# Performance work log

Hardware: AMD Instinct MI355X
Metric: run time of the kernel (lower is better)

## Reference

```python
import jax, jax.numpy as jnp
import numpy as np

B, T, INPUT_DIM = 4, 2048, 1024
N_HEADS, HEAD_DIM, EMB_DIM = 16, 64, 1024


def setup_inputs() -> dict:
    key = jax.random.key(0)
    ks = jax.random.split(key, 7)
    s = 0.02
    return {
        "k": jax.random.normal(ks[0], (B, T, INPUT_DIM), jnp.float32),
        "q": jax.random.normal(ks[1], (B, T, INPUT_DIM), jnp.float32),
        "v": jax.random.normal(ks[2], (B, T, INPUT_DIM), jnp.float32),
        # weights stored [in, out] (torch Linear applies x @ W.T with W [out,in])
        "w_key": jax.random.normal(ks[3], (INPUT_DIM, N_HEADS * HEAD_DIM), jnp.float32) * s,
        "w_query": jax.random.normal(ks[4], (INPUT_DIM, N_HEADS * HEAD_DIM), jnp.float32) * s,
        "w_value": jax.random.normal(ks[5], (INPUT_DIM, N_HEADS * HEAD_DIM), jnp.float32) * s,
        "w_proj": jax.random.normal(ks[6], (N_HEADS * HEAD_DIM, EMB_DIM), jnp.float32) * s,
    }


def reference(k, q, v, w_key, w_query, w_value, w_proj):
    temperature = np.sqrt(HEAD_DIM).astype(np.float32)
    # projections -> [B, T, H, D]
    kh = (k @ w_key).reshape(B, T, N_HEADS, HEAD_DIM)
    qh = (q @ w_query).reshape(B, T, N_HEADS, HEAD_DIM)
    vh = (v @ w_value).reshape(B, T, N_HEADS, HEAD_DIM)
    # scaled dot-product attention: scores [B, H, T, T]
    scores = jnp.einsum("bqhd,bkhd->bhqk", qh, kh) / temperature
    attn = jax.nn.softmax(scores, axis=-1)
    out = jnp.einsum("bhqk,bkhd->bqhd", attn, vh).reshape(B, T, N_HEADS * HEAD_DIM)
    return out @ w_proj
```

## Files before the change

### kernel.cpp

```cpp
#include <hip/hip_runtime.h>

typedef unsigned short bf16_t;
typedef __attribute__((ext_vector_type(8))) short short8;
typedef __attribute__((ext_vector_type(4))) float f32x4;
typedef __attribute__((ext_vector_type(16))) float f32x16;
typedef __attribute__((ext_vector_type(4))) unsigned short usx4;

#define T_SEQ 2048
#define NHEAD 16

__device__ __forceinline__ unsigned short f2bf(float x) {
  union { float f; unsigned u; } v; v.f = x;
  unsigned r = v.u + 0x7fffu + ((v.u >> 16) & 1u);
  return (unsigned short)(r >> 16);
}

__device__ __forceinline__ void gld_lds16(const void* g, void* l) {
  __builtin_amdgcn_global_load_lds((const __attribute__((address_space(1))) void*)g,
                                   (__attribute__((address_space(3))) void*)l, 16, 0, 0);
}

__device__ __forceinline__ unsigned cvtpk(float lo, float hi) {
  unsigned r;
  asm("v_cvt_pk_bf16_f32 %0, %1, %2" : "=v"(r) : "v"(lo), "v"(hi));
  return r;
}

__global__ __launch_bounds__(256) void cvt3(const float* __restrict__ a,
                                            const float* __restrict__ b,
                                            const float* __restrict__ c,
                                            bf16_t* __restrict__ oa,
                                            bf16_t* __restrict__ ob,
                                            bf16_t* __restrict__ oc, int n4seg) {
  int i = blockIdx.x * 256 + threadIdx.x;
  const int stride = gridDim.x * 256;
  const int total = 3 * n4seg;
  for (; i < total; i += stride) {
    const int seg = i / n4seg;
    const int j = i - seg * n4seg;
    const float* in = (seg == 0) ? a : (seg == 1) ? b : c;
    bf16_t* out = (seg == 0) ? oa : (seg == 1) ? ob : oc;
    const float4 v = ((const float4*)in)[j];
    usx4 w = { f2bf(v.x), f2bf(v.y), f2bf(v.z), f2bf(v.w) };
    ((usx4*)out)[j] = w;
  }
}

__global__ __launch_bounds__(256) void wtrans(const float* __restrict__ w0, const float* __restrict__ w1,
                                              const float* __restrict__ w2, const float* __restrict__ w3,
                                              bf16_t* __restrict__ wt) {
  __shared__ float tile[32][33];
  const float* w = (blockIdx.z == 0) ? w0 : (blockIdx.z == 1) ? w1 : (blockIdx.z == 2) ? w2 : w3;
  bf16_t* o = wt + (size_t)blockIdx.z * 1024 * 1024;
  const int c = threadIdx.x & 31;
  const int r = threadIdx.x >> 5;
  const int k0 = blockIdx.y * 32, n0 = blockIdx.x * 32;
#pragma unroll
  for (int rr = 0; rr < 32; rr += 8)
    tile[r + rr][c] = w[(size_t)(k0 + r + rr) * 1024 + n0 + c];
  __syncthreads();
#pragma unroll
  for (int rr = 0; rr < 32; rr += 8)
    o[(size_t)(n0 + r + rr) * 1024 + k0 + c] = f2bf(tile[c][r + rr]);
}

__global__ __launch_bounds__(256) void gemm_qkv(const bf16_t* __restrict__ A0,
                                                const bf16_t* __restrict__ A1,
                                                const bf16_t* __restrict__ A2,
                                                const bf16_t* __restrict__ Wt,
                                                bf16_t* __restrict__ C0,
                                                bf16_t* __restrict__ C1,
                                                bf16_t* __restrict__ C2) {
  __shared__ bf16_t As[2][128 * 64];
  __shared__ bf16_t Bs[2][128 * 64];
  const int K = 1024;
  const int z = blockIdx.z;
  const bf16_t* A  = (z == 0) ? A0 : (z == 1) ? A1 : A2;
  const bf16_t* Bt = Wt + (size_t)z * 1024 * 1024;
  const int tid = threadIdx.x;
  const int lane = tid & 63;
  const int l15 = lane & 15;
  const int g = lane >> 4;
  const int wave = tid >> 6;
  const int wr = wave >> 1, wc = wave & 1;
  const int f = blockIdx.x + (int)gridDim.x * blockIdx.y;
  const int fp = (f & 7) * 64 + (f >> 3);
  const int col0 = (fp & 7) * 128, row0 = (fp >> 3) * 128;

  f32x4 acc[4][4];
#pragma unroll
  for (int m = 0; m < 4; ++m)
#pragma unroll
    for (int n = 0; n < 4; ++n) acc[m][n] = (f32x4){0.f, 0.f, 0.f, 0.f};

  const int r_st = tid >> 3;
  const int c_st = tid & 7;

  auto stage = [&](int kt, int bi) {
#pragma unroll
    for (int i = 0; i < 4; ++i) {
      const int r = r_st + i * 32;
      gld_lds16(A  + (size_t)(row0 + r) * K + kt + c_st * 8, As[bi] + (size_t)(tid + i * 256) * 8);
      gld_lds16(Bt + (size_t)(col0 + r) * K + kt + c_st * 8, Bs[bi] + (size_t)(tid + i * 256) * 8);
    }
  };

  const int NIT = K / 64;
  stage(0, 0);
  stage(64, 1);

  for (int it = 0; it < NIT; ++it) {
    const int cur = it & 1;
    if (it + 1 < NIT) { asm volatile("s_waitcnt vmcnt(8)" ::: "memory"); }
    else              { asm volatile("s_waitcnt vmcnt(0)" ::: "memory"); }
    __builtin_amdgcn_s_barrier();
    __builtin_amdgcn_sched_barrier(0);
#pragma unroll
    for (int ks = 0; ks < 2; ++ks) {
      short8 a[4], b[4];
#pragma unroll
      for (int m = 0; m < 4; ++m)
        a[m] = *(const short8*)(As[cur] + (wr * 64 + m * 16 + l15) * 64 + ks * 32 + g * 8);
#pragma unroll
      for (int n = 0; n < 4; ++n)
        b[n] = *(const short8*)(Bs[cur] + (wc * 64 + n * 16 + l15) * 64 + ks * 32 + g * 8);
#pragma unroll
      for (int m = 0; m < 4; ++m)
#pragma unroll
        for (int n = 0; n < 4; ++n)
          acc[m][n] = __builtin_amdgcn_mfma_f32_16x16x32_bf16(a[m], b[n], acc[m][n], 0, 0, 0);
    }
    __builtin_amdgcn_s_barrier();
    __builtin_amdgcn_sched_barrier(0);
    if (it + 2 < NIT) stage((it + 2) * 64, cur);
  }

  if (z == 2) {
#pragma unroll
    for (int m = 0; m < 4; ++m) {
      const int row = row0 + wr * 64 + m * 16 + g * 4;
      const int bb = row >> 11;
      const int t = row & 2047;
#pragma unroll
      for (int n = 0; n < 4; ++n) {
        const int col = col0 + wc * 64 + n * 16 + l15;
        const int hh = col >> 6, dd = col & 63;
        usx4 w = { f2bf(acc[m][n][0]), f2bf(acc[m][n][1]), f2bf(acc[m][n][2]), f2bf(acc[m][n][3]) };
        *(usx4*)(C2 + (((size_t)(bb * 16 + hh) * 64 + dd) * 2048 + t)) = w;
      }
    }
  } else {
    const float sc = (z == 1) ? 0.18033688011112042f : 1.0f;
    bf16_t* C = (z == 1) ? C1 : C0;
#pragma unroll
    for (int m = 0; m < 4; ++m) {
      const int row = row0 + wr * 64 + m * 16 + g * 4;
#pragma unroll
      for (int n = 0; n < 4; ++n) {
        const int col = col0 + wc * 64 + n * 16 + l15;
#pragma unroll
        for (int i = 0; i < 4; ++i)
          C[(size_t)(row + i) * 1024 + col] = f2bf(acc[m][n][i] * sc);
      }
    }
  }
}

__global__ __launch_bounds__(256) void gemm_proj(const bf16_t* __restrict__ A,
                                                 const bf16_t* __restrict__ Bt,
                                                 float* __restrict__ C, int K) {
  __shared__ bf16_t As[2][128 * 64];
  __shared__ bf16_t Bs[2][128 * 64];
  const int tid = threadIdx.x;
  const int lane = tid & 63;
  const int l15 = lane & 15;
  const int g = lane >> 4;
  const int wave = tid >> 6;
  const int wr = wave >> 1, wc = wave & 1;
  const int f = blockIdx.x + (int)gridDim.x * blockIdx.y;
  const int fp = (f & 7) * 64 + (f >> 3);
  const int col0 = (fp & 7) * 128, row0 = (fp >> 3) * 128;

  f32x4 acc[4][4];
#pragma unroll
  for (int m = 0; m < 4; ++m)
#pragma unroll
    for (int n = 0; n < 4; ++n) acc[m][n] = (f32x4){0.f, 0.f, 0.f, 0.f};

  const int r_st = tid >> 3;
  const int c_st = tid & 7;

  auto stage = [&](int kt, int bi) {
#pragma unroll
    for (int i = 0; i < 4; ++i) {
      const int r = r_st + i * 32;
      gld_lds16(A  + (size_t)(row0 + r) * K + kt + c_st * 8, As[bi] + (size_t)(tid + i * 256) * 8);
      gld_lds16(Bt + (size_t)(col0 + r) * K + kt + c_st * 8, Bs[bi] + (size_t)(tid + i * 256) * 8);
    }
  };

  const int NIT = K / 64;
  stage(0, 0);
  stage(64, 1);

  for (int it = 0; it < NIT; ++it) {
    const int cur = it & 1;
    if (it + 1 < NIT) { asm volatile("s_waitcnt vmcnt(8)" ::: "memory"); }
    else              { asm volatile("s_waitcnt vmcnt(0)" ::: "memory"); }
    __builtin_amdgcn_s_barrier();
    __builtin_amdgcn_sched_barrier(0);
#pragma unroll
    for (int ks = 0; ks < 2; ++ks) {
      short8 a[4], b[4];
#pragma unroll
      for (int m = 0; m < 4; ++m)
        a[m] = *(const short8*)(As[cur] + (wr * 64 + m * 16 + l15) * 64 + ks * 32 + g * 8);
#pragma unroll
      for (int n = 0; n < 4; ++n)
        b[n] = *(const short8*)(Bs[cur] + (wc * 64 + n * 16 + l15) * 64 + ks * 32 + g * 8);
#pragma unroll
      for (int m = 0; m < 4; ++m)
#pragma unroll
        for (int n = 0; n < 4; ++n)
          acc[m][n] = __builtin_amdgcn_mfma_f32_16x16x32_bf16(a[m], b[n], acc[m][n], 0, 0, 0);
    }
    __builtin_amdgcn_s_barrier();
    __builtin_amdgcn_sched_barrier(0);
    if (it + 2 < NIT) stage((it + 2) * 64, cur);
  }

#pragma unroll
  for (int m = 0; m < 4; ++m) {
    const int row = row0 + wr * 64 + m * 16 + g * 4;
#pragma unroll
    for (int n = 0; n < 4; ++n) {
      const int col = col0 + wc * 64 + n * 16 + l15;
#pragma unroll
      for (int i = 0; i < 4; ++i)
        C[(size_t)(row + i) * 1024 + col] = acc[m][n][i];
    }
  }
}

__global__ __launch_bounds__(256) void attn_fwd(const bf16_t* __restrict__ qh,
                                                const bf16_t* __restrict__ kh,
                                                const bf16_t* __restrict__ vt,
                                                bf16_t* __restrict__ ao) {
  __shared__ bf16_t smem[16384];
  const int tid = threadIdx.x;
  const int lane = tid & 63;
  const int l31 = lane & 31;
  const int half = lane >> 5;
  const int wave = tid >> 6;
  const int f = blockIdx.x + (int)gridDim.x * blockIdx.y;
  const int fp = (f & 7) * 128 + (f >> 3);
  const int qblk = fp & 15;
  const int bh = fp >> 4;
  const int b = bh >> 4, h = bh & 15;

  const int tq = qblk * 128 + wave * 32 + l31;
  const size_t qoff = (size_t)(b * T_SEQ + tq) * 1024 + h * 64;
  short8 qf[4];
#pragma unroll
  for (int ks = 0; ks < 4; ++ks)
    qf[ks] = *(const short8*)(qh + qoff + ks * 16 + half * 8);

  union { short8 v; unsigned u[4]; } onesf;
#pragma unroll
  for (int i = 0; i < 4; ++i) onesf.u[i] = 0x3F803F80u;

  f32x16 ov0, ov1, lacc;
#pragma unroll
  for (int i = 0; i < 16; ++i) { ov0[i] = 0.f; ov1[i] = 0.f; lacc[i] = 0.f; }

  const size_t kbase = (size_t)b * T_SEQ * 1024 + h * 64;
  const size_t vbase = (size_t)bh * 64 * T_SEQ;
  const int r_st = tid >> 3;
  const int cd = tid & 7;

  auto stage = [&](int kvt, int bufi) {
    bf16_t* Ks = smem + bufi * 8192;
    bf16_t* Vs = Ks + 4096;
    const int t0 = kvt * 64;
#pragma unroll
    for (int i = 0; i < 2; ++i) {
      const int r = r_st + i * 32;
      const int cs = cd ^ (r & 7);
      gld_lds16(kh + kbase + (size_t)(t0 + r) * 1024 + cs * 8, Ks + (size_t)(tid + i * 256) * 8);
      gld_lds16(vt + vbase + (size_t)r * T_SEQ + t0 + cs * 8,  Vs + (size_t)(tid + i * 256) * 8);
    }
  };

  const int NT = T_SEQ / 64;
  stage(0, 0);
  stage(1, 1);

  for (int kv = 0; kv < NT; ++kv) {
    const int cur = kv & 1;
    if (kv + 1 < NT) { asm volatile("s_waitcnt vmcnt(4)" ::: "memory"); }
    else             { asm volatile("s_waitcnt vmcnt(0)" ::: "memory"); }
    __builtin_amdgcn_s_barrier();
    __builtin_amdgcn_sched_barrier(0);
    const bf16_t* Ks = smem + cur * 8192;
    const bf16_t* Vs = Ks + 4096;

    f32x16 st[2];
#pragma unroll
    for (int t = 0; t < 2; ++t)
#pragma unroll
      for (int i = 0; i < 16; ++i) st[t][i] = 0.f;
    __builtin_amdgcn_s_setprio(1);
#pragma unroll
    for (int t = 0; t < 2; ++t) {
      const int row = t * 32 + l31;
#pragma unroll
      for (int ks = 0; ks < 4; ++ks) {
        const short8 af = *(const short8*)(Ks + row * 64 + (((ks * 2 + half) ^ (l31 & 7)) * 8));
        st[t] = __builtin_amdgcn_mfma_f32_32x32x16_bf16(af, qf[ks], st[t], 0, 0, 0);
      }
    }
    __builtin_amdgcn_s_setprio(0);

#pragma unroll
    for (int t = 0; t < 2; ++t)
#pragma unroll
      for (int i = 0; i < 16; ++i)
        st[t][i] = __builtin_amdgcn_exp2f(st[t][i]);

#pragma unroll
    for (int s = 0; s < 4; ++s) {
      const int t = s >> 1, base = (s & 1) * 8;
      unsigned c0 = cvtpk(st[t][base + 0], st[t][base + 1]);
      unsigned c1 = cvtpk(st[t][base + 2], st[t][base + 3]);
      unsigned c2 = cvtpk(st[t][base + 4], st[t][base + 5]);
      unsigned c3 = cvtpk(st[t][base + 6], st[t][base + 7]);
      asm("v_permlane32_swap_b32 %0, %1" : "+v"(c0), "+v"(c2));
      asm("v_permlane32_swap_b32 %0, %1" : "+v"(c1), "+v"(c3));
      union { short8 v; unsigned u[4]; } bu;
      bu.u[0] = c0; bu.u[1] = c1; bu.u[2] = c2; bu.u[3] = c3;
      __builtin_amdgcn_s_setprio(1);
      lacc = __builtin_amdgcn_mfma_f32_32x32x16_bf16(onesf.v, bu.v, lacc, 0, 0, 0);
#pragma unroll
      for (int dt = 0; dt < 2; ++dt) {
        const int row = dt * 32 + l31;
        const short8 av = *(const short8*)(Vs + row * 64 + (((s * 2 + half) ^ (l31 & 7)) * 8));
        if (dt == 0) ov0 = __builtin_amdgcn_mfma_f32_32x32x16_bf16(av, bu.v, ov0, 0, 0, 0);
        else         ov1 = __builtin_amdgcn_mfma_f32_32x32x16_bf16(av, bu.v, ov1, 0, 0, 0);
      }
      __builtin_amdgcn_s_setprio(0);
    }
    __builtin_amdgcn_s_barrier();
    __builtin_amdgcn_sched_barrier(0);
    if (kv + 2 < NT) stage(kv + 2, cur);
  }

  const float inv = 1.f / lacc[0];
  bf16_t* obuf = smem + wave * 2048;
#pragma unroll
  for (int k = 0; k < 4; ++k) {
    usx4 w0 = { f2bf(ov0[4 * k + 0] * inv), f2bf(ov0[4 * k + 1] * inv),
                f2bf(ov0[4 * k + 2] * inv), f2bf(ov0[4 * k + 3] * inv) };
    *(usx4*)(obuf + l31 * 64 + ((k ^ (l31 & 7)) * 8) + half * 4) = w0;
    usx4 w1 = { f2bf(ov1[4 * k + 0] * inv), f2bf(ov1[4 * k + 1] * inv),
                f2bf(ov1[4 * k + 2] * inv), f2bf(ov1[4 * k + 3] * inv) };
    *(usx4*)(obuf + l31 * 64 + (((4 + k) ^ (l31 & 7)) * 8) + half * 4) = w1;
  }
  __syncthreads();
  const int r = lane >> 1;
  const int cb = (lane & 1) * 4;
  const size_t orow = (size_t)(b * T_SEQ + qblk * 128 + wave * 32 + r) * 1024 + h * 64;
#pragma unroll
  for (int c = 0; c < 4; ++c) {
    const int ch = cb + c;
    const short8 v = *(const short8*)(obuf + r * 64 + ((ch ^ (r & 7)) * 8));
    *(short8*)(ao + orow + ch * 8) = v;
  }
}

extern "C" void kernel_launch(void* const* d_in, const int* in_sizes, int n_in,
                              void* d_out, int out_size, void* d_ws, size_t ws_size,
                              hipStream_t stream) {
  const float* k_in  = (const float*)d_in[0];
  const float* q_in  = (const float*)d_in[1];
  const float* v_in  = (const float*)d_in[2];
  const float* w_key = (const float*)d_in[3];
  const float* w_qry = (const float*)d_in[4];
  const float* w_val = (const float*)d_in[5];
  const float* w_prj = (const float*)d_in[6];

  char* ws = (char*)d_ws;
  bf16_t* xb0 = (bf16_t*)(ws);
  bf16_t* xb1 = (bf16_t*)(ws + (16u << 20));
  bf16_t* xb2 = (bf16_t*)(ws + (32u << 20));
  bf16_t* wt  = (bf16_t*)(ws + (48u << 20));
  bf16_t* qh  = (bf16_t*)(ws + (56u << 20));
  bf16_t* kh  = (bf16_t*)(ws + (72u << 20));
  bf16_t* vt  = (bf16_t*)(ws + (88u << 20));
  bf16_t* ao  = (bf16_t*)(ws);

  wtrans<<<dim3(32, 32, 4), 256, 0, stream>>>(w_key, w_qry, w_val, w_prj, wt);

  const int N4 = (8192 * 1024) / 4;
  cvt3<<<3072, 256, 0, stream>>>(k_in, q_in, v_in, xb0, xb1, xb2, N4);

  gemm_qkv<<<dim3(8, 64, 3), 256, 0, stream>>>(xb0, xb1, xb2, wt, kh, qh, vt);

  attn_fwd<<<dim3(16, 64), 256, 0, stream>>>(qh, kh, vt, ao);

  gemm_proj<<<dim3(8, 64), 256, 0, stream>>>(ao, wt + 3u * (1u << 20), (float*)d_out, 1024);
}
```

Before: 227.0 us.

## Triple-buffer K/V tiles in attention to drop the second per-iteration barrier

The attention loop moves from two to three LDS buffers for K/V tiles. The next-next tile is issued right after the top barrier into the free third buffer, so the trailing barrier before restaging is removed and the loads overlap the whole compute. It also precomputes swizzled LDS offsets and seeds the first QK MFMA from a zero vector, dropping the per-tile accumulator zeroing. LDS use grows from 32KB to 48KB per block, which may lower occupancy, and an extra full vmcnt(0) wait is added before the loop.

```diff
diff --git a/kernel.cpp b/kernel.cpp
--- a/kernel.cpp
+++ b/kernel.cpp
@@ -246,7 +246,7 @@
                                                 const bf16_t* __restrict__ kh,
                                                 const bf16_t* __restrict__ vt,
                                                 bf16_t* __restrict__ ao) {
-  __shared__ bf16_t smem[16384];
+  __shared__ bf16_t smem[24576];
   const int tid = threadIdx.x;
   const int lane = tid & 63;
   const int l31 = lane & 31;
@@ -269,53 +269,62 @@
 #pragma unroll
   for (int i = 0; i < 4; ++i) onesf.u[i] = 0x3F803F80u;
 
-  f32x16 ov0, ov1, lacc;
-#pragma unroll
-  for (int i = 0; i < 16; ++i) { ov0[i] = 0.f; ov1[i] = 0.f; lacc[i] = 0.f; }
+  f32x16 ov0, ov1, lacc, zv;
+#pragma unroll
+  for (int i = 0; i < 16; ++i) { ov0[i] = 0.f; ov1[i] = 0.f; lacc[i] = 0.f; zv[i] = 0.f; }
+
+  int off[2][4];
+#pragma unroll
+  for (int k = 0; k < 4; ++k) {
+    const int swz = ((k * 2 + half) ^ (l31 & 7)) * 8;
+    off[0][k] = l31 * 64 + swz;
+    off[1][k] = (32 + l31) * 64 + swz;
+  }
 
   const size_t kbase = (size_t)b * T_SEQ * 1024 + h * 64;
   const size_t vbase = (size_t)bh * 64 * T_SEQ;
   const int r_st = tid >> 3;
   const int cd = tid & 7;
 
-  auto stage = [&](int kvt, int bufi) {
-    bf16_t* Ks = smem + bufi * 8192;
-    bf16_t* Vs = Ks + 4096;
+  bf16_t* p0 = smem;
+  bf16_t* p1 = smem + 8192;
+  bf16_t* p2 = smem + 16384;
+
+  auto stage = [&](int kvt, bf16_t* buf) {
     const int t0 = kvt * 64;
 #pragma unroll
     for (int i = 0; i < 2; ++i) {
       const int r = r_st + i * 32;
       const int cs = cd ^ (r & 7);
-      gld_lds16(kh + kbase + (size_t)(t0 + r) * 1024 + cs * 8, Ks + (size_t)(tid + i * 256) * 8);
-      gld_lds16(vt + vbase + (size_t)r * T_SEQ + t0 + cs * 8,  Vs + (size_t)(tid + i * 256) * 8);
+      gld_lds16(kh + kbase + (size_t)(t0 + r) * 1024 + cs * 8, buf + (size_t)(tid + i * 256) * 8);
+      gld_lds16(vt + vbase + (size_t)r * T_SEQ + t0 + cs * 8,  buf + 4096 + (size_t)(tid + i * 256) * 8);
     }
   };
 
   const int NT = T_SEQ / 64;
-  stage(0, 0);
-  stage(1, 1);
+  stage(0, p0);
+  stage(1, p1);
+  asm volatile("s_waitcnt vmcnt(0)" ::: "memory");
 
   for (int kv = 0; kv < NT; ++kv) {
-    const int cur = kv & 1;
     if (kv + 1 < NT) { asm volatile("s_waitcnt vmcnt(4)" ::: "memory"); }
     else             { asm volatile("s_waitcnt vmcnt(0)" ::: "memory"); }
     __builtin_amdgcn_s_barrier();
     __builtin_amdgcn_sched_barrier(0);
-    const bf16_t* Ks = smem + cur * 8192;
-    const bf16_t* Vs = Ks + 4096;
+    if (kv + 2 < NT) stage(kv + 2, p2);
+
+    const bf16_t* Ks = p0;
+    const bf16_t* Vs = p0 + 4096;
 
     f32x16 st[2];
-#pragma unroll
-    for (int t = 0; t < 2; ++t)
-#pragma unroll
-      for (int i = 0; i < 16; ++i) st[t][i] = 0.f;
     __builtin_amdgcn_s_setprio(1);
 #pragma unroll
     for (int t = 0; t < 2; ++t) {
-      const int row = t * 32 + l31;
-#pragma unroll
-      for (int ks = 0; ks < 4; ++ks) {
-        const short8 af = *(const short8*)(Ks + row * 64 + (((ks * 2 + half) ^ (l31 & 7)) * 8));
+      const short8 af0 = *(const short8*)(Ks + off[t][0]);
+      st[t] = __builtin_amdgcn_mfma_f32_32x32x16_bf16(af0, qf[0], zv, 0, 0, 0);
+#pragma unroll
+      for (int ks = 1; ks < 4; ++ks) {
+        const short8 af = *(const short8*)(Ks + off[t][ks]);
         st[t] = __builtin_amdgcn_mfma_f32_32x32x16_bf16(af, qf[ks], st[t], 0, 0, 0);
       }
     }
@@ -340,18 +349,14 @@
       bu.u[0] = c0; bu.u[1] = c1; bu.u[2] = c2; bu.u[3] = c3;
       __builtin_amdgcn_s_setprio(1);
       lacc = __builtin_amdgcn_mfma_f32_32x32x16_bf16(onesf.v, bu.v, lacc, 0, 0, 0);
-#pragma unroll
-      for (int dt = 0; dt < 2; ++dt) {
-        const int row = dt * 32 + l31;
-        const short8 av = *(const short8*)(Vs + row * 64 + (((s * 2 + half) ^ (l31 & 7)) * 8));
-        if (dt == 0) ov0 = __builtin_amdgcn_mfma_f32_32x32x16_bf16(av, bu.v, ov0, 0, 0, 0);
-        else         ov1 = __builtin_amdgcn_mfma_f32_32x32x16_bf16(av, bu.v, ov1, 0, 0, 0);
-      }
+      const short8 av0 = *(const short8*)(Vs + off[0][s]);
+      ov0 = __builtin_amdgcn_mfma_f32_32x32x16_bf16(av0, bu.v, ov0, 0, 0, 0);
+      const short8 av1 = *(const short8*)(Vs + off[1][s]);
+      ov1 = __builtin_amdgcn_mfma_f32_32x32x16_bf16(av1, bu.v, ov1, 0, 0, 0);
       __builtin_amdgcn_s_setprio(0);
     }
-    __builtin_amdgcn_s_barrier();
-    __builtin_amdgcn_sched_barrier(0);
-    if (kv + 2 < NT) stage(kv + 2, cur);
+
+    bf16_t* tmp = p0; p0 = p1; p1 = p2; p2 = tmp;
   }
 
   const float inv = 1.f / lacc[0];
```

After: 226.8 us (median of 3 runs). About the same (-0.1%).
